# Kernel optimization log

Hardware: AMD Instinct MI355X
Metric: run time of the kernel (lower is better)

The kernel has to match this reference:

```python
import jax, jax.numpy as jnp
import numpy as np
from jax import lax

EPS = 1e-5  # BatchNorm eps (eval mode, running stats)
HEADS = 8

# --- surrogate-gradient Heaviside (sigmoid surrogate, alpha=4) ---
@jax.custom_vjp
def spike(u):
    return (u >= 0.0).astype(u.dtype)

def _spike_fwd(u):
    return spike(u), u

def _spike_bwd(u, g):
    s = jax.nn.sigmoid(4.0 * u)
    return (g * 4.0 * s * (1.0 - s),)

spike.defvjp(_spike_fwd, _spike_bwd)

def lif(x, tau=0.5, threshold=1.0):
    """Multi-step LIF over leading time axis: v_t = tau*v_{t-1} + x_t,
    s_t = H(v_t - threshold), hard reset v_t *= (1 - s_t)."""
    def step(v, xt):
        v = tau * v + xt
        s = spike(v - threshold)
        return v * (1.0 - s), s
    _, out = lax.scan(step, jnp.zeros_like(x[0]), x)
    return out

def bn_eval(x, gamma, beta, mean, var):
    # x: (T,B,C,N); per-channel affine using running stats
    inv = gamma / jnp.sqrt(var + EPS)
    return x * inv[None, None, :, None] + (beta - mean * inv)[None, None, :, None]

def setup_inputs() -> dict:
    key = jax.random.key(0)
    ks = jax.random.split(key, 12)
    T, B, C, H, W = 4, 32, 384, 16, 16
    d = {}
    d['x'] = jax.random.normal(ks[0], (T, B, C, H, W), dtype=jnp.float32)
    # 1x1 Conv1d weights == (C_out, C_in) matrices
    sc = 1.0 / np.sqrt(C)
    d['q_w'] = jax.random.normal(ks[1], (C, C), dtype=jnp.float32) * sc
    d['q_gamma'] = jnp.ones((C,), jnp.float32)
    d['q_beta'] = jnp.zeros((C,), jnp.float32)
    d['q_mean'] = jax.random.normal(ks[2], (C,), dtype=jnp.float32) * 0.1
    d['q_var'] = jax.random.uniform(ks[3], (C,), dtype=jnp.float32) + 0.5
    d['k_w'] = jax.random.normal(ks[4], (C, C), dtype=jnp.float32) * sc
    d['k_gamma'] = jnp.ones((C,), jnp.float32)
    d['k_beta'] = jnp.zeros((C,), jnp.float32)
    d['k_mean'] = jax.random.normal(ks[5], (C,), dtype=jnp.float32) * 0.1
    d['k_var'] = jax.random.uniform(ks[6], (C,), dtype=jnp.float32) + 0.5
    d['proj_w'] = jax.random.normal(ks[7], (C, C), dtype=jnp.float32) * sc
    d['proj_b'] = jax.random.normal(ks[8], (C,), dtype=jnp.float32) * 0.01
    d['proj_gamma'] = jnp.ones((C,), jnp.float32)
    d['proj_beta'] = jnp.zeros((C,), jnp.float32)
    d['proj_mean'] = jax.random.normal(ks[9], (C,), dtype=jnp.float32) * 0.1
    d['proj_var'] = jax.random.uniform(ks[10], (C,), dtype=jnp.float32) + 0.5
    d['mem_alpha'] = jnp.float32(0.2)
    return d

def reference(x, q_w, q_gamma, q_beta, q_mean, q_var,
              k_w, k_gamma, k_beta, k_mean, k_var,
              proj_w, proj_b, proj_gamma, proj_beta, proj_mean, proj_var,
              mem_alpha):
    T, B, C, H, W = x.shape
    Hh = HEADS
    Dh = C // Hh
    N = H * W
    # proj_lif applied to raw input, then flatten spatial dims
    s = lif(x, tau=0.5, threshold=1.0).reshape(T, B, C, N)
    # q path: 1x1 conv (channel GEMM) -> BN -> LIF
    q = lif(bn_eval(jnp.einsum('tbcn,dc->tbdn', s, q_w), q_gamma, q_beta, q_mean, q_var),
            tau=0.5, threshold=1.0).reshape(T, B, Hh, Dh, N)
    # k path
    k = lif(bn_eval(jnp.einsum('tbcn,dc->tbdn', s, k_w), k_gamma, k_beta, k_mean, k_var),
            tau=0.5, threshold=1.0).reshape(T, B, Hh, Dh, N)
    # temporal decayed memory: m_0 = q_0; m_t = alpha*m_{t-1} + (1-alpha)*q_{t-1}
    def mstep(m_prev, q_prev):
        m = mem_alpha * m_prev + (1.0 - mem_alpha) * q_prev
        return m, m
    _, mems_rest = lax.scan(mstep, q[0], q[:-1])
    mems = jnp.concatenate([q[:1], mems_rest], axis=0)  # (T,B,Hh,Dh,N)
    # cat along Dh then sum == sum(mems)+sum(q)
    q_sum = jnp.sum(mems, axis=3, keepdims=True) + jnp.sum(q, axis=3, keepdims=True)
    attn = lif(q_sum, tau=0.5, threshold=0.5)  # (T,B,Hh,1,N)
    y = (attn * k).reshape(T, B, C, N)
    # proj conv (with bias) -> BN -> reshape back to (T,B,C,H,W)
    y = jnp.einsum('tbcn,dc->tbdn', y, proj_w) + proj_b[None, None, :, None]
    y = bn_eval(y, proj_gamma, proj_beta, proj_mean, proj_var)
    return y.reshape(T, B, C, H, W)
```

## Files before the change

kernel.cpp:

```cpp
#include <hip/hip_runtime.h>

#define T_ 4
#define B_ 32
#define C_ 384
#define N_ 256
#define HEADS_ 8
#define DH_ 48
#define EPS_ 1e-5f
#define NW_ (C_*C_)

typedef _Float16 f16;
typedef __attribute__((ext_vector_type(8))) _Float16 f16x8;
typedef __attribute__((ext_vector_type(16))) float f32x16;

#define PSCALE     4096.0f
#define PSCALE_INV (1.0f/4096.0f)

__global__ __launch_bounds__(256)
void prep_kernel(const float* __restrict__ x, f16* __restrict__ s,
                 const float* __restrict__ qw, const float* __restrict__ kw,
                 const float* __restrict__ pw,
                 f16* __restrict__ q2, f16* __restrict__ k2, f16* __restrict__ p2)
{
    if (blockIdx.z == 32) {
        const int base = (blockIdx.y * 4 + blockIdx.x) * 256 + threadIdx.x;
        int idx = base;
#pragma unroll 4
        for (int it = 0; it < 48; ++it) {
            {
                float w = qw[idx]; f16 a = (f16)w; f16 bb = (f16)((w - (float)a) * PSCALE);
                q2[idx] = a; q2[NW_ + idx] = bb;
            }
            {
                float w = kw[idx]; f16 a = (f16)w; f16 bb = (f16)((w - (float)a) * PSCALE);
                k2[idx] = a; k2[NW_ + idx] = bb;
            }
            {
                float w = pw[idx]; f16 a = (f16)w; f16 bb = (f16)((w - (float)a) * PSCALE);
                p2[idx] = a; p2[NW_ + idx] = bb;
            }
            idx += 3072;
        }
        return;
    }

    const int tid = threadIdx.x;
    const int ng = tid & 15;
    const int cg = tid >> 4;
    const int n4 = blockIdx.x * 64 + ng * 4;
    const int c0 = blockIdx.y * 128 + cg * 8;
    const int b  = blockIdx.z;

    float v[8][4];
#pragma unroll
    for (int i = 0; i < 8; ++i)
#pragma unroll
        for (int j = 0; j < 4; ++j) v[i][j] = 0.f;

#pragma unroll
    for (int t = 0; t < T_; ++t) {
        const float* xt = x + (((size_t)t * B_ + b) * C_) * N_;
        float4 xv[8];
#pragma unroll
        for (int i = 0; i < 8; ++i)
            xv[i] = *(const float4*)&xt[(size_t)(c0 + i) * N_ + n4];
#pragma unroll
        for (int j = 0; j < 4; ++j) {
            union { f16 h[8]; uint4 q; } u;
#pragma unroll
            for (int i = 0; i < 8; ++i) {
                float xa = (j == 0) ? xv[i].x : (j == 1) ? xv[i].y
                         : (j == 2) ? xv[i].z : xv[i].w;
                float vv = 0.5f * v[i][j] + xa;
                int sp = (vv >= 1.0f) ? 1 : 0;
                v[i][j] = sp ? 0.f : vv;
                u.h[i] = sp ? (f16)1.0f : (f16)0.0f;
            }
            f16* dst = s + (((size_t)t * B_ + b) * N_ + n4 + j) * (size_t)C_ + c0;
            *(uint4*)dst = u.q;
        }
    }
}

__global__ __launch_bounds__(256)
void qk_gemm_lif_kernel(const f16* __restrict__ Wq, const f16* __restrict__ Wk,
                        const f16* __restrict__ S,
                        const float* __restrict__ qg, const float* __restrict__ qb,
                        const float* __restrict__ qm, const float* __restrict__ qv,
                        const float* __restrict__ kg, const float* __restrict__ kb,
                        const float* __restrict__ km, const float* __restrict__ kv,
                        f16* __restrict__ q_spk, f16* __restrict__ k_spk)
{
    __shared__ __align__(16) char smem[36864];
    f16 (*As)[72]      = reinterpret_cast<f16(*)[72]>(smem);
    f16 (*Bs)[64][72]  = reinterpret_cast<f16(*)[64][72]>(smem + 18432);

    const int tid  = threadIdx.x;
    const int lane = tid & 63;
    const int wave = tid >> 6;
    const int wm = wave & 1, wd = wave >> 1;
    const int l31 = lane & 31;
    const int lhi = lane >> 5;

    const int path = blockIdx.x & 1;
    const int mb = blockIdx.x >> 1;
    const int b  = mb >> 3;
    const int n0 = (mb & 7) * 32;
    const int d0 = blockIdx.y * 64;

    const f16* W = path ? Wk : Wq;
    const float* g_  = path ? kg : qg;
    const float* be_ = path ? kb : qb;
    const float* m_  = path ? km : qm;
    const float* va_ = path ? kv : qv;
    f16* spk = path ? k_spk : q_spk;

    const int dcol = d0 + wd * 32 + l31;
    const float inv = g_[dcol] / sqrtf(va_[dcol] + EPS_);
    const float add = be_[dcol] - m_[dcol] * inv;

    const int ar = tid >> 1;
    const int ah = (tid & 1) * 32;
    const f16* arow = S + (((size_t)(ar & 3) * B_ + b) * N_ + n0 + (ar >> 2)) * (size_t)C_;

    const int bp = tid >> 7;
    const int brr = (tid >> 1) & 63;
    const int bh = (tid & 1) * 32;
    const f16* brow = W + (size_t)bp * NW_ + (size_t)(d0 + brr) * C_;

    f32x16 acc[2][2];
#pragma unroll
    for (int ms = 0; ms < 2; ++ms)
#pragma unroll
        for (int p = 0; p < 2; ++p)
#pragma unroll
            for (int r = 0; r < 16; ++r) acc[ms][p][r] = 0.f;

    for (int kc = 0; kc < C_; kc += 64) {
        __syncthreads();
        {
            const f16* ga = arow + kc + ah;
            *(uint4*)&As[ar][ah]      = *(const uint4*)(ga);
            *(uint4*)&As[ar][ah + 8]  = *(const uint4*)(ga + 8);
            *(uint4*)&As[ar][ah + 16] = *(const uint4*)(ga + 16);
            *(uint4*)&As[ar][ah + 24] = *(const uint4*)(ga + 24);
            const f16* gb = brow + kc + bh;
            *(uint4*)&Bs[bp][brr][bh]      = *(const uint4*)(gb);
            *(uint4*)&Bs[bp][brr][bh + 8]  = *(const uint4*)(gb + 8);
            *(uint4*)&Bs[bp][brr][bh + 16] = *(const uint4*)(gb + 16);
            *(uint4*)&Bs[bp][brr][bh + 24] = *(const uint4*)(gb + 24);
        }
        __syncthreads();
#pragma unroll
        for (int kk = 0; kk < 4; ++kk) {
            const int ko = kk * 16 + lhi * 8;
            f16x8 a0 = *(const f16x8*)&As[wm * 64 + l31][ko];
            f16x8 a1 = *(const f16x8*)&As[wm * 64 + 32 + l31][ko];
            f16x8 b0 = *(const f16x8*)&Bs[0][wd * 32 + l31][ko];
            f16x8 b1 = *(const f16x8*)&Bs[1][wd * 32 + l31][ko];
            acc[0][0] = __builtin_amdgcn_mfma_f32_32x32x16_f16(a0, b0, acc[0][0], 0, 0, 0);
            acc[1][0] = __builtin_amdgcn_mfma_f32_32x32x16_f16(a1, b0, acc[1][0], 0, 0, 0);
            acc[0][1] = __builtin_amdgcn_mfma_f32_32x32x16_f16(a0, b1, acc[0][1], 0, 0, 0);
            acc[1][1] = __builtin_amdgcn_mfma_f32_32x32x16_f16(a1, b1, acc[1][1], 0, 0, 0);
        }
    }

#pragma unroll
    for (int ms = 0; ms < 2; ++ms)
#pragma unroll
    for (int g = 0; g < 4; ++g) {
        const int n = n0 + wm * 16 + ms * 8 + 2 * g + lhi;
        float v = 0.f;
#pragma unroll
        for (int t = 0; t < 4; ++t) {
            const int r = g * 4 + t;
            float val = (acc[ms][0][r] + acc[ms][1][r] * PSCALE_INV) * inv + add;
            float vv = 0.5f * v + val;
            int sp = (vv >= 1.0f) ? 1 : 0;
            v = sp ? 0.f : vv;
            spk[(((size_t)t * B_ + b) * N_ + n) * C_ + dcol] =
                sp ? (f16)1.0f : (f16)0.0f;
        }
    }
}

__global__ __launch_bounds__(256)
void head_attn_kernel(const f16* __restrict__ q_spk,
                      const float* __restrict__ alpha_p,
                      unsigned char* __restrict__ attn)
{
    int i = blockIdx.x * 256 + threadIdx.x;
    int n = i & (N_ - 1);
    int h = (i >> 8) & (HEADS_ - 1);
    int b = i >> 11;
    const float alpha = alpha_p[0];
    const int stride = B_ * HEADS_ * N_;
    float M = 0.f, v = 0.f, Sprev = 0.f;
#pragma unroll
    for (int t = 0; t < T_; ++t) {
        const uint4* p = (const uint4*)(q_spk + (((size_t)(t * B_ + b) * N_) + n) * C_ + h * DH_);
        int cnt = 0;
#pragma unroll
        for (int j = 0; j < 6; ++j) {
            uint4 w = p[j];
            cnt += __popc(w.x & 0x04000400u) + __popc(w.y & 0x04000400u)
                 + __popc(w.z & 0x04000400u) + __popc(w.w & 0x04000400u);
        }
        float Sqt = (float)cnt;
        if (t == 0) M = Sqt;
        else        M = alpha * M + (1.f - alpha) * Sprev;
        float qsum = M + Sqt;
        float vv = 0.5f * v + qsum;
        unsigned char sp = (vv >= 0.5f) ? 1 : 0;
        v = sp ? 0.f : vv;
        attn[(size_t)t * stride + i] = sp;
        Sprev = Sqt;
    }
}

__global__ __launch_bounds__(256)
void proj_gemm_kernel(const f16* __restrict__ Wp,
                      const f16* __restrict__ K,
                      const unsigned char* __restrict__ attn,
                      const float* __restrict__ bias,
                      const float* __restrict__ gamma, const float* __restrict__ beta,
                      const float* __restrict__ mean,  const float* __restrict__ var,
                      float* __restrict__ out)
{
    __shared__ __align__(16) char smem[36864];
    f16 (*As)[72]     = reinterpret_cast<f16(*)[72]>(smem);
    f16 (*Bs)[64][72] = reinterpret_cast<f16(*)[64][72]>(smem + 18432);

    const int tid  = threadIdx.x;
    const int lane = tid & 63;
    const int wave = tid >> 6;
    const int wm = wave & 1, wd = wave >> 1;
    const int l31 = lane & 31;
    const int lhi = lane >> 5;

    const int mb = blockIdx.x;
    const int tb = mb >> 1;
    const int n0 = (mb & 1) * 128;
    const int d0 = blockIdx.y * 64;

    const int dcol = d0 + wd * 32 + l31;
    const float iv = gamma[dcol] / sqrtf(var[dcol] + EPS_);
    const float ad = beta[dcol] - mean[dcol] * iv + bias[dcol] * iv;

    const int ar = tid >> 1;
    const int ah = (tid & 1) * 32;
    const int an = n0 + ar;
    const f16* arow = K + ((size_t)tb * N_ + an) * (size_t)C_;
    const unsigned char* At = attn + (size_t)tb * HEADS_ * N_;

    const int bp = tid >> 7;
    const int brr = (tid >> 1) & 63;
    const int bh = (tid & 1) * 32;
    const f16* brow = Wp + (size_t)bp * NW_ + (size_t)(d0 + brr) * C_;

    f32x16 acc[2][2];
#pragma unroll
    for (int ms = 0; ms < 2; ++ms)
#pragma unroll
        for (int p = 0; p < 2; ++p)
#pragma unroll
            for (int r = 0; r < 16; ++r) acc[ms][p][r] = 0.f;

    for (int kc = 0; kc < C_; kc += 64) {
        __syncthreads();
        {
#pragma unroll
            for (int j = 0; j < 4; ++j) {
                int c = kc + ah + 8 * j;
                int h = c / DH_;
                unsigned char am = At[(size_t)h * N_ + an];
                uint4 val = am ? *(const uint4*)(arow + c) : make_uint4(0u, 0u, 0u, 0u);
                *(uint4*)&As[ar][ah + 8 * j] = val;
            }
            const f16* gb = brow + kc + bh;
            *(uint4*)&Bs[bp][brr][bh]      = *(const uint4*)(gb);
            *(uint4*)&Bs[bp][brr][bh + 8]  = *(const uint4*)(gb + 8);
            *(uint4*)&Bs[bp][brr][bh + 16] = *(const uint4*)(gb + 16);
            *(uint4*)&Bs[bp][brr][bh + 24] = *(const uint4*)(gb + 24);
        }
        __syncthreads();
#pragma unroll
        for (int kk = 0; kk < 4; ++kk) {
            const int ko = kk * 16 + lhi * 8;
            f16x8 a0 = *(const f16x8*)&As[wm * 64 + l31][ko];
            f16x8 a1 = *(const f16x8*)&As[wm * 64 + 32 + l31][ko];
            f16x8 b0 = *(const f16x8*)&Bs[0][wd * 32 + l31][ko];
            f16x8 b1 = *(const f16x8*)&Bs[1][wd * 32 + l31][ko];
            acc[0][0] = __builtin_amdgcn_mfma_f32_32x32x16_f16(a0, b0, acc[0][0], 0, 0, 0);
            acc[1][0] = __builtin_amdgcn_mfma_f32_32x32x16_f16(a1, b0, acc[1][0], 0, 0, 0);
            acc[0][1] = __builtin_amdgcn_mfma_f32_32x32x16_f16(a0, b1, acc[0][1], 0, 0, 0);
            acc[1][1] = __builtin_amdgcn_mfma_f32_32x32x16_f16(a1, b1, acc[1][1], 0, 0, 0);
        }
    }

    float* obase = out + ((size_t)tb * C_ + dcol) * N_;
#pragma unroll
    for (int ms = 0; ms < 2; ++ms)
#pragma unroll
    for (int r = 0; r < 16; ++r) {
        int n = n0 + wm * 64 + ms * 32 + (r & 3) + 8 * (r >> 2) + 4 * lhi;
        float val = acc[ms][0][r] + acc[ms][1][r] * PSCALE_INV;
        obase[n] = val * iv + ad;
    }
}

extern "C" void kernel_launch(void* const* d_in, const int* in_sizes, int n_in,
                              void* d_out, int out_size, void* d_ws, size_t ws_size,
                              hipStream_t stream)
{
    const float* x       = (const float*)d_in[0];
    const float* q_w     = (const float*)d_in[1];
    const float* q_gamma = (const float*)d_in[2];
    const float* q_beta  = (const float*)d_in[3];
    const float* q_mean  = (const float*)d_in[4];
    const float* q_var   = (const float*)d_in[5];
    const float* k_w     = (const float*)d_in[6];
    const float* k_gamma = (const float*)d_in[7];
    const float* k_beta  = (const float*)d_in[8];
    const float* k_mean  = (const float*)d_in[9];
    const float* k_var   = (const float*)d_in[10];
    const float* proj_w  = (const float*)d_in[11];
    const float* proj_b  = (const float*)d_in[12];
    const float* p_gamma = (const float*)d_in[13];
    const float* p_beta  = (const float*)d_in[14];
    const float* p_mean  = (const float*)d_in[15];
    const float* p_var   = (const float*)d_in[16];
    const float* m_alpha = (const float*)d_in[17];

    float* out = (float*)d_out;

    const size_t SPK_BYTES = (size_t)T_ * B_ * N_ * C_ * sizeof(f16);
    const size_t W2_BYTES  = (size_t)2 * NW_ * sizeof(f16);
    const size_t TBHN      = (size_t)T_ * B_ * HEADS_ * N_;

    unsigned char* ws = (unsigned char*)d_ws;
    size_t off = 0;
    auto carve = [&](size_t bytes) {
        off = (off + 255) & ~(size_t)255;
        void* p = ws + off;
        off += bytes;
        return p;
    };
    f16* s_f16  = (f16*)carve(SPK_BYTES);
    f16* q_spk  = (f16*)carve(SPK_BYTES);
    f16* k_spk  = (f16*)carve(SPK_BYTES);
    f16* Wq2    = (f16*)carve(W2_BYTES);
    f16* Wk2    = (f16*)carve(W2_BYTES);
    f16* Wp2    = (f16*)carve(W2_BYTES);
    unsigned char* attn = (unsigned char*)carve(TBHN);

    dim3 pgrid1(4, 3, 33);
    prep_kernel<<<pgrid1, 256, 0, stream>>>(x, s_f16, q_w, k_w, proj_w,
                                            Wq2, Wk2, Wp2);

    dim3 qkgrid(512, 6);
    qk_gemm_lif_kernel<<<qkgrid, 256, 0, stream>>>(Wq2, Wk2, s_f16,
                                                   q_gamma, q_beta, q_mean, q_var,
                                                   k_gamma, k_beta, k_mean, k_var,
                                                   q_spk, k_spk);

    head_attn_kernel<<<(B_ * HEADS_ * N_) / 256, 256, 0, stream>>>(q_spk, m_alpha, attn);

    dim3 pjgrid(256, 6);
    proj_gemm_kernel<<<pjgrid, 256, 0, stream>>>(Wp2, k_spk, attn, proj_b,
                                                 p_gamma, p_beta, p_mean, p_var, out);
}
```

Baseline: 230.8 us.

## Store q/k spikes as bytes and unpack to fp16 in proj GEMM loads

The q and k spike tensors are written as single bytes (0x3C, the high byte of fp16 1.0) instead of fp16, halving their write and read traffic. The head-attention popcount reads half as many words, and the projection GEMM loads 8 bytes and expands them to fp16 with byte-permute instructions before the LDS store. The qk GEMM grid is rearranged so q/k paths are split along grid y, and the A tile row mapping changes to a time-major layout with matching LDS read pointers. The trade-off is extra unpack ALU work in the projection load path.

```diff
diff --git a/kernel.cpp b/kernel.cpp
--- a/kernel.cpp
+++ b/kernel.cpp
@@ -15,6 +15,17 @@
 
 #define PSCALE     4096.0f
 #define PSCALE_INV (1.0f/4096.0f)
+#define SPIKE_BYTE 0x3Cu
+
+__device__ __forceinline__ void unpack4(unsigned int w, unsigned int& lo, unsigned int& hi) {
+#if defined(__has_builtin) && __has_builtin(__builtin_amdgcn_perm)
+    lo = __builtin_amdgcn_perm(w, w, 0x010C000Cu);
+    hi = __builtin_amdgcn_perm(w, w, 0x030C020Cu);
+#else
+    lo = ((w & 0xFFu) << 8) | ((w & 0xFF00u) << 16);
+    hi = ((w & 0x00FF0000u) >> 8) | (w & 0xFF000000u);
+#endif
+}
 
 __global__ __launch_bounds__(256)
 void prep_kernel(const float* __restrict__ x, f16* __restrict__ s,
@@ -89,7 +100,8 @@
                         const float* __restrict__ qm, const float* __restrict__ qv,
                         const float* __restrict__ kg, const float* __restrict__ kb,
                         const float* __restrict__ km, const float* __restrict__ kv,
-                        f16* __restrict__ q_spk, f16* __restrict__ k_spk)
+                        unsigned char* __restrict__ q_spk,
+                        unsigned char* __restrict__ k_spk)
 {
     __shared__ __align__(16) char smem[36864];
     f16 (*As)[72]      = reinterpret_cast<f16(*)[72]>(smem);
@@ -102,18 +114,19 @@
     const int l31 = lane & 31;
     const int lhi = lane >> 5;
 
-    const int path = blockIdx.x & 1;
-    const int mb = blockIdx.x >> 1;
+    const int mb = blockIdx.x;
     const int b  = mb >> 3;
     const int n0 = (mb & 7) * 32;
-    const int d0 = blockIdx.y * 64;
+    const int dp0 = blockIdx.y * 64;
+    const int path = (dp0 >= C_) ? 1 : 0;
+    const int d0 = dp0 - path * C_;
 
     const f16* W = path ? Wk : Wq;
     const float* g_  = path ? kg : qg;
     const float* be_ = path ? kb : qb;
     const float* m_  = path ? km : qm;
     const float* va_ = path ? kv : qv;
-    f16* spk = path ? k_spk : q_spk;
+    unsigned char* spk = path ? k_spk : q_spk;
 
     const int dcol = d0 + wd * 32 + l31;
     const float inv = g_[dcol] / sqrtf(va_[dcol] + EPS_);
@@ -121,12 +134,17 @@
 
     const int ar = tid >> 1;
     const int ah = (tid & 1) * 32;
-    const f16* arow = S + (((size_t)(ar & 3) * B_ + b) * N_ + n0 + (ar >> 2)) * (size_t)C_;
+    const int at = ar >> 5;
+    const int an = n0 + (ar & 31);
+    const f16* arow = S + (((size_t)at * B_ + b) * N_ + an) * (size_t)C_;
 
     const int bp = tid >> 7;
     const int brr = (tid >> 1) & 63;
     const int bh = (tid & 1) * 32;
     const f16* brow = W + (size_t)bp * NW_ + (size_t)(d0 + brr) * C_;
+
+    const f16* pa0 = &As[32 * (l31 & 3) + wm * 16 + (l31 >> 2)][0];
+    const f16* pa1 = pa0 + 8 * 72;
 
     f32x16 acc[2][2];
 #pragma unroll
@@ -154,8 +172,8 @@
 #pragma unroll
         for (int kk = 0; kk < 4; ++kk) {
             const int ko = kk * 16 + lhi * 8;
-            f16x8 a0 = *(const f16x8*)&As[wm * 64 + l31][ko];
-            f16x8 a1 = *(const f16x8*)&As[wm * 64 + 32 + l31][ko];
+            f16x8 a0 = *(const f16x8*)(pa0 + ko);
+            f16x8 a1 = *(const f16x8*)(pa1 + ko);
             f16x8 b0 = *(const f16x8*)&Bs[0][wd * 32 + l31][ko];
             f16x8 b1 = *(const f16x8*)&Bs[1][wd * 32 + l31][ko];
             acc[0][0] = __builtin_amdgcn_mfma_f32_32x32x16_f16(a0, b0, acc[0][0], 0, 0, 0);
@@ -179,13 +197,13 @@
             int sp = (vv >= 1.0f) ? 1 : 0;
             v = sp ? 0.f : vv;
             spk[(((size_t)t * B_ + b) * N_ + n) * C_ + dcol] =
-                sp ? (f16)1.0f : (f16)0.0f;
+                sp ? (unsigned char)SPIKE_BYTE : (unsigned char)0;
         }
     }
 }
 
 __global__ __launch_bounds__(256)
-void head_attn_kernel(const f16* __restrict__ q_spk,
+void head_attn_kernel(const unsigned char* __restrict__ q_spk,
                       const float* __restrict__ alpha_p,
                       unsigned char* __restrict__ attn)
 {
@@ -201,10 +219,10 @@
         const uint4* p = (const uint4*)(q_spk + (((size_t)(t * B_ + b) * N_) + n) * C_ + h * DH_);
         int cnt = 0;
 #pragma unroll
-        for (int j = 0; j < 6; ++j) {
+        for (int j = 0; j < 3; ++j) {
             uint4 w = p[j];
-            cnt += __popc(w.x & 0x04000400u) + __popc(w.y & 0x04000400u)
-                 + __popc(w.z & 0x04000400u) + __popc(w.w & 0x04000400u);
+            cnt += __popc(w.x & 0x04040404u) + __popc(w.y & 0x04040404u)
+                 + __popc(w.z & 0x04040404u) + __popc(w.w & 0x04040404u);
         }
         float Sqt = (float)cnt;
         if (t == 0) M = Sqt;
@@ -220,7 +238,7 @@
 
 __global__ __launch_bounds__(256)
 void proj_gemm_kernel(const f16* __restrict__ Wp,
-                      const f16* __restrict__ K,
+                      const unsigned char* __restrict__ K8,
                       const unsigned char* __restrict__ attn,
                       const float* __restrict__ bias,
                       const float* __restrict__ gamma, const float* __restrict__ beta,
@@ -250,7 +268,7 @@
     const int ar = tid >> 1;
     const int ah = (tid & 1) * 32;
     const int an = n0 + ar;
-    const f16* arow = K + ((size_t)tb * N_ + an) * (size_t)C_;
+    const unsigned char* arow = K8 + ((size_t)tb * N_ + an) * (size_t)C_;
     const unsigned char* At = attn + (size_t)tb * HEADS_ * N_;
 
     const int bp = tid >> 7;
@@ -274,8 +292,11 @@
                 int c = kc + ah + 8 * j;
                 int h = c / DH_;
                 unsigned char am = At[(size_t)h * N_ + an];
-                uint4 val = am ? *(const uint4*)(arow + c) : make_uint4(0u, 0u, 0u, 0u);
-                *(uint4*)&As[ar][ah + 8 * j] = val;
+                uint2 w2 = am ? *(const uint2*)(arow + c) : make_uint2(0u, 0u);
+                uint4 o;
+                unpack4(w2.x, o.x, o.y);
+                unpack4(w2.y, o.z, o.w);
+                *(uint4*)&As[ar][ah + 8 * j] = o;
             }
             const f16* gb = brow + kc + bh;
             *(uint4*)&Bs[bp][brr][bh]      = *(const uint4*)(gb);
@@ -334,7 +355,8 @@
 
     float* out = (float*)d_out;
 
-    const size_t SPK_BYTES = (size_t)T_ * B_ * N_ * C_ * sizeof(f16);
+    const size_t S_BYTES   = (size_t)T_ * B_ * N_ * C_ * sizeof(f16);
+    const size_t SPK_BYTES = (size_t)T_ * B_ * N_ * C_;
     const size_t W2_BYTES  = (size_t)2 * NW_ * sizeof(f16);
     const size_t TBHN      = (size_t)T_ * B_ * HEADS_ * N_;
 
@@ -346,9 +368,9 @@
         off += bytes;
         return p;
     };
-    f16* s_f16  = (f16*)carve(SPK_BYTES);
-    f16* q_spk  = (f16*)carve(SPK_BYTES);
-    f16* k_spk  = (f16*)carve(SPK_BYTES);
+    f16* s_f16  = (f16*)carve(S_BYTES);
+    unsigned char* q_spk = (unsigned char*)carve(SPK_BYTES);
+    unsigned char* k_spk = (unsigned char*)carve(SPK_BYTES);
     f16* Wq2    = (f16*)carve(W2_BYTES);
     f16* Wk2    = (f16*)carve(W2_BYTES);
     f16* Wp2    = (f16*)carve(W2_BYTES);
@@ -358,7 +380,7 @@
     prep_kernel<<<pgrid1, 256, 0, stream>>>(x, s_f16, q_w, k_w, proj_w,
                                             Wq2, Wk2, Wp2);
 
-    dim3 qkgrid(512, 6);
+    dim3 qkgrid(256, 12);
     qk_gemm_lif_kernel<<<qkgrid, 256, 0, stream>>>(Wq2, Wk2, s_f16,
                                                    q_gamma, q_beta, q_mean, q_var,
                                                    k_gamma, k_beta, k_mean, k_var,
```

Result: no change. 228.1 us (-1.2%).
